# Performance work log

Hardware: AMD Instinct MI355X
Metric: run time of the kernel (lower is better)

The kernel has to match this reference:

```python
import jax, jax.numpy as jnp
import numpy as np

HEIGHT = 480
K = 16
RADIUS = 5.0 / HEIGHT


def ball_query_idx(xy, radius, k):
    """pytorch3d-style ball_query on 2D points (t-channel is zeroed in the
    original, so 3D distance == 2D distance on (x, y)).
    Returns first-k (in point-index order) neighbor indices within radius;
    slots with no neighbor are filled with the query's own index (the
    module's `-1 -> self` replacement).  xy: [B, N, 2] -> idx: [B, N, k] int32."""
    B, N, _ = xy.shape
    sq = jnp.sum(xy * xy, axis=-1)  # [B, N]
    # d2[b, i, j] = ||xy[b,i] - xy[b,j]||^2, via GEMM (no [B,N,N,2] intermediate)
    d2 = sq[:, :, None] + sq[:, None, :] - 2.0 * jnp.einsum('bnd,bmd->bnm', xy, xy)
    within = d2 < radius * radius  # [B, N, N]
    ar = jnp.arange(N, dtype=jnp.int32)
    # key = j if within else N; k smallest keys == first k neighbors in index order
    keys = jnp.where(within, ar[None, None, :], N)
    neg_top, _ = jax.lax.top_k(-keys, k)  # k smallest keys, ascending after negate
    idx = -neg_top  # [B, N, k]
    self_idx = jnp.broadcast_to(ar[None, :, None], (B, N, k))
    return jnp.where(idx < N, idx, self_idx)


def knn_gather(x, idx):
    # x: [B, N, D], idx: [B, N, k] -> [B, N, k, D]
    return jax.vmap(lambda xb, ib: xb[ib])(x, idx)


def setup_inputs() -> dict:
    key = jax.random.key(0)
    k1, k2, k3 = jax.random.split(key, 3)
    B, N = 8, 4096
    out_ch = 64
    hid = out_ch * 2          # 128
    in_ch = K * 2             # 32
    xytp = jax.random.uniform(k1, (B, N, 4), dtype=jnp.float32)
    W1 = jax.random.normal(k2, (in_ch, hid), dtype=jnp.float32) / np.sqrt(in_ch)
    b1 = jnp.zeros((hid,), dtype=jnp.float32)
    W2 = jax.random.normal(k3, (hid, out_ch), dtype=jnp.float32) / np.sqrt(hid)
    b2 = jnp.zeros((out_ch,), dtype=jnp.float32)
    return {"xytp": xytp, "W1": W1, "b1": b1, "W2": W2, "b2": b2}


def reference(xytp, W1, b1, W2, b2):
    xy = xytp[..., 1:3]  # [B, N, 2]
    # ball query runs on detached coords in the original
    idx = ball_query_idx(jax.lax.stop_gradient(xy), RADIUS, K)  # [B, N, K]
    delta = xy[:, :, None, :] - knn_gather(xy, idx)  # [B, N, K, 2]
    B, N = delta.shape[:2]
    emb = delta.reshape(B, N, K * 2)  # [B, N, 2K]
    h = jax.nn.relu(emb @ W1 + b1)
    return h @ W2 + b2  # [B, N, out_channel]
```

## Files before the change

kernel.cpp:

```cpp
#include <hip/hip_runtime.h>

#define NB    8
#define NPTS  4096
#define KNN   16
#define CG    16
#define NCC   (CG * CG)
#define PCAP  24

#define R2F ((float)((5.0 / 480.0) * (5.0 / 480.0)))
#define WIN 0.011f

__global__ __launch_bounds__(1024, 8) void k_all(
    const float4* __restrict__ xytp4, const float* __restrict__ W1,
    const float* __restrict__ b1, const float* __restrict__ W2,
    const float* __restrict__ b2, float* __restrict__ out) {
#pragma clang fp contract(off)
  __shared__ __align__(16) char smemA[32768];
  __shared__ unsigned short csrIdx[4096];
  __shared__ int offs[NCC + 1];
  __shared__ int cellcnt[NCC];
  __shared__ unsigned int plist[64 * PCAP];
  __shared__ int pcnt[64];
  __shared__ unsigned short idxposT[KNN][64];
  __shared__ float embT[32][64];

  float* csrX = (float*)smemA;
  float* csrY = (float*)(smemA + 16384);
  float(*hsT)[64] = (float(*)[64])smemA;

  const int t = threadIdx.x;
  const int p = t & 63;
  const int q = t >> 6;
  const int pbase = blockIdx.x * 64;
  const int bb = pbase & ~4095;
  const int lqbase = pbase & 4095;

  float4 Preg[4];
  int cellreg[4];
#pragma unroll
  for (int r = 0; r < 4; ++r) Preg[r] = xytp4[bb + t + 1024 * r];
  if (t < NCC) cellcnt[t] = 0;
  __syncthreads();
#pragma unroll
  for (int r = 0; r < 4; ++r) {
    int cx = min(CG - 1, max(0, (int)(Preg[r].y * (float)CG)));
    int cy = min(CG - 1, max(0, (int)(Preg[r].z * (float)CG)));
    cellreg[r] = cy * CG + cx;
    atomicAdd(&cellcnt[cellreg[r]], 1);
  }
  __syncthreads();

  if (q == 0) {
    int b4 = p * 4;
    int s0 = cellcnt[b4], s1 = cellcnt[b4 + 1], s2 = cellcnt[b4 + 2],
        s3 = cellcnt[b4 + 3];
    int tot = s0 + s1 + s2 + s3;
    int inc = tot;
#pragma unroll
    for (int d = 1; d < 64; d <<= 1) {
      int up = __shfl_up(inc, d);
      if (p >= d) inc += up;
    }
    int ex = inc - tot;
    offs[b4] = ex; offs[b4 + 1] = ex + s0;
    offs[b4 + 2] = ex + s0 + s1; offs[b4 + 3] = ex + s0 + s1 + s2;
    if (p == 63) offs[NCC] = inc;
    cellcnt[b4] = ex; cellcnt[b4 + 1] = ex + s0;
    cellcnt[b4 + 2] = ex + s0 + s1; cellcnt[b4 + 3] = ex + s0 + s1 + s2;
  }
  __syncthreads();

#pragma unroll
  for (int r = 0; r < 4; ++r) {
    int pos = atomicAdd(&cellcnt[cellreg[r]], 1);
    csrX[pos] = Preg[r].y; csrY[pos] = Preg[r].z;
    csrIdx[pos] = (unsigned short)(t + 1024 * r);
  }
  __syncthreads();

  {
    const int q0 = q * 4;
    const unsigned long long below = (1ull << p) - 1;
#pragma unroll
    for (int g = 0; g < 4; ++g) {
      int lq = q0 + g;
      float4 P = xytp4[pbase + lq];
      float xn = P.y, yn = P.z;
      float sqn = xn * xn + yn * yn;
      int cxlo = max(0, (int)((xn - WIN) * (float)CG));
      int cxhi = min(CG - 1, (int)((xn + WIN) * (float)CG));
      int cylo = max(0, (int)((yn - WIN) * (float)CG));
      int cyhi = min(CG - 1, (int)((yn + WIN) * (float)CG));
      int cnt = 0;
      for (int cy_ = cylo; cy_ <= cyhi; ++cy_)
        for (int cx_ = cxlo; cx_ <= cxhi; ++cx_) {
          int cell = cy_ * CG + cx_;
          int st = offs[cell], en = offs[cell + 1];
          for (int base = st; base < en; base += 64) {
            int e = base + p;
            bool act = e < en;
            int ee = act ? e : st;
            float cx2 = csrX[ee], cy2 = csrY[ee];
            float cs2 = cx2 * cx2 + cy2 * cy2;
            float tt = fmaf(yn, cy2, xn * cx2);
            float d = (sqn + cs2) - (tt + tt);
            bool pass = act && (d < R2F);
            unsigned long long mask = __ballot(pass);
            if (pass) {
              int slot = cnt + __popcll(mask & below);
              if (slot < PCAP)
                plist[lq * PCAP + slot] =
                    ((unsigned int)csrIdx[ee] << 12) | (unsigned int)ee;
            }
            cnt += __popcll(mask);
          }
        }
      if (p == 0) pcnt[lq] = cnt;
    }
  }
  __syncthreads();

  if (t < 64) {
    int c = min(pcnt[t], PCAP);
    unsigned int* cand = &plist[t * PCAP];
    for (int i = 1; i < c; ++i) {
      unsigned int key = cand[i];
      int j = i - 1;
      while (j >= 0 && cand[j] > key) { cand[j + 1] = cand[j]; --j; }
      cand[j + 1] = key;
    }
    unsigned short selfPos = 0;
    if (c < KNN) {
      unsigned int selfIdx = (unsigned int)(lqbase + t);
      for (int i = 0; i < c; ++i)
        if ((cand[i] >> 12) == selfIdx) { selfPos = cand[i] & 4095u; break; }
    }
    if (c > KNN) c = KNN;
    for (int k = 0; k < KNN; ++k)
      idxposT[k][t] =
          (k < c) ? (unsigned short)(cand[k] & 4095u) : selfPos;
  }
  __syncthreads();

  {
    float4 Pq = xytp4[pbase + p];
    int m = idxposT[q][p];
    embT[2 * q][p] = Pq.y - csrX[m];
    embT[2 * q + 1][p] = Pq.z - csrY[m];
  }
  __syncthreads();

  {
    const int u0 = __builtin_amdgcn_readfirstlane(q) * 8;
    float h[8];
#pragma unroll
    for (int j = 0; j < 8; ++j) h[j] = b1[u0 + j];
#pragma unroll
    for (int k = 0; k < 32; ++k) {
      float ek = embT[k][p];
      const float* __restrict__ w0 = W1 + k * 128 + u0;
#pragma unroll
      for (int j = 0; j < 8; ++j) h[j] = fmaf(ek, w0[j], h[j]);
    }
#pragma unroll
    for (int j = 0; j < 8; ++j)
      hsT[u0 + j][p] = fmaxf(h[j], 0.f);
  }
  __syncthreads();

  {
    const int o0 = __builtin_amdgcn_readfirstlane(q) * 4;
    float acc[4];
#pragma unroll
    for (int j = 0; j < 4; ++j) acc[j] = b2[o0 + j];
#pragma unroll 8
    for (int g = 0; g < 64; ++g) {
      float h0 = hsT[2 * g][p];
      float h1 = hsT[2 * g + 1][p];
      const float* __restrict__ w0 = W2 + (2 * g) * 64 + o0;
#pragma unroll
      for (int j = 0; j < 4; ++j) acc[j] = fmaf(h0, w0[j], acc[j]);
#pragma unroll
      for (int j = 0; j < 4; ++j) acc[j] = fmaf(h1, w0[64 + j], acc[j]);
    }
    *(float4*)(out + (size_t)(pbase + p) * 64 + o0) =
        make_float4(acc[0], acc[1], acc[2], acc[3]);
  }
}

extern "C" void kernel_launch(void* const* d_in, const int* in_sizes, int n_in,
                              void* d_out, int out_size, void* d_ws, size_t ws_size,
                              hipStream_t stream) {
  const float4* xytp4 = (const float4*)d_in[0];
  const float* W1 = (const float*)d_in[1];
  const float* b1 = (const float*)d_in[2];
  const float* W2 = (const float*)d_in[3];
  const float* b2 = (const float*)d_in[4];
  float* out = (float*)d_out;
  (void)d_ws; (void)ws_size;

  hipLaunchKernelGGL(k_all, dim3(512), dim3(1024), 0, stream, xytp4, W1, b1,
                     W2, b2, out);
}
```

Measured before the change: 86.65 us.

## Split grid CSR build into a separate per-batch kernel shared by all blocks

Moves the spatial grid counting, prefix scan and CSR scatter into a new kernel that runs once per batch and writes cell offsets and sorted points to workspace. The main kernel then just loads the prebuilt CSR into shared memory instead of every block rebuilding it. This removes work repeated 64 times per batch, at the cost of an extra kernel launch, a serialized 8-block build stage, and global memory round-trips.

Measured after the change: 89.45 us. 1.03x slower.

```diff
diff --git a/kernel.cpp b/kernel.cpp
--- a/kernel.cpp
+++ b/kernel.cpp
@@ -10,15 +10,75 @@
 #define R2F ((float)((5.0 / 480.0) * (5.0 / 480.0)))
 #define WIN 0.011f
 
-__global__ __launch_bounds__(1024, 8) void k_all(
-    const float4* __restrict__ xytp4, const float* __restrict__ W1,
+#define WS_CSR 0x10000
+
+__global__ __launch_bounds__(1024) void k_build(
+    const float4* __restrict__ xytp4, int* __restrict__ offs_g,
+    float4* __restrict__ csr_g) {
+#pragma clang fp contract(off)
+  __shared__ int offs[NCC + 1];
+  __shared__ int cellcnt[NCC];
+
+  const int t = threadIdx.x;
+  const int p = t & 63;
+  const int q = t >> 6;
+  const int b = blockIdx.x;
+  const int bb = b << 12;
+
+  float4 Preg[4];
+  int cellreg[4];
+#pragma unroll
+  for (int r = 0; r < 4; ++r) Preg[r] = xytp4[bb + t + 1024 * r];
+  if (t < NCC) cellcnt[t] = 0;
+  __syncthreads();
+#pragma unroll
+  for (int r = 0; r < 4; ++r) {
+    int cx = min(CG - 1, max(0, (int)(Preg[r].y * (float)CG)));
+    int cy = min(CG - 1, max(0, (int)(Preg[r].z * (float)CG)));
+    cellreg[r] = cy * CG + cx;
+    atomicAdd(&cellcnt[cellreg[r]], 1);
+  }
+  __syncthreads();
+
+  if (q == 0) {
+    int b4 = p * 4;
+    int s0 = cellcnt[b4], s1 = cellcnt[b4 + 1], s2 = cellcnt[b4 + 2],
+        s3 = cellcnt[b4 + 3];
+    int tot = s0 + s1 + s2 + s3;
+    int inc = tot;
+#pragma unroll
+    for (int d = 1; d < 64; d <<= 1) {
+      int up = __shfl_up(inc, d);
+      if (p >= d) inc += up;
+    }
+    int ex = inc - tot;
+    offs[b4] = ex; offs[b4 + 1] = ex + s0;
+    offs[b4 + 2] = ex + s0 + s1; offs[b4 + 3] = ex + s0 + s1 + s2;
+    if (p == 63) offs[NCC] = inc;
+    cellcnt[b4] = ex; cellcnt[b4 + 1] = ex + s0;
+    cellcnt[b4 + 2] = ex + s0 + s1; cellcnt[b4 + 3] = ex + s0 + s1 + s2;
+  }
+  __syncthreads();
+
+#pragma unroll
+  for (int r = 0; r < 4; ++r) {
+    int pos = atomicAdd(&cellcnt[cellreg[r]], 1);
+    csr_g[(b << 12) + pos] =
+        make_float4(Preg[r].y, Preg[r].z,
+                    __uint_as_float((unsigned)(t + 1024 * r)), 0.f);
+  }
+  if (t < NCC + 1) offs_g[b * (NCC + 1) + t] = offs[t];
+}
+
+__global__ __launch_bounds__(1024, 8) void k_main(
+    const float4* __restrict__ xytp4, const int* __restrict__ offs_g,
+    const float4* __restrict__ csr_g, const float* __restrict__ W1,
     const float* __restrict__ b1, const float* __restrict__ W2,
     const float* __restrict__ b2, float* __restrict__ out) {
 #pragma clang fp contract(off)
   __shared__ __align__(16) char smemA[32768];
   __shared__ unsigned short csrIdx[4096];
   __shared__ int offs[NCC + 1];
-  __shared__ int cellcnt[NCC];
   __shared__ unsigned int plist[64 * PCAP];
   __shared__ int pcnt[64];
   __shared__ unsigned short idxposT[KNN][64];
@@ -32,50 +92,17 @@
   const int p = t & 63;
   const int q = t >> 6;
   const int pbase = blockIdx.x * 64;
-  const int bb = pbase & ~4095;
+  const int b = pbase >> 12;
   const int lqbase = pbase & 4095;
 
-  float4 Preg[4];
-  int cellreg[4];
-#pragma unroll
-  for (int r = 0; r < 4; ++r) Preg[r] = xytp4[bb + t + 1024 * r];
-  if (t < NCC) cellcnt[t] = 0;
-  __syncthreads();
 #pragma unroll
   for (int r = 0; r < 4; ++r) {
-    int cx = min(CG - 1, max(0, (int)(Preg[r].y * (float)CG)));
-    int cy = min(CG - 1, max(0, (int)(Preg[r].z * (float)CG)));
-    cellreg[r] = cy * CG + cx;
-    atomicAdd(&cellcnt[cellreg[r]], 1);
-  }
-  __syncthreads();
-
-  if (q == 0) {
-    int b4 = p * 4;
-    int s0 = cellcnt[b4], s1 = cellcnt[b4 + 1], s2 = cellcnt[b4 + 2],
-        s3 = cellcnt[b4 + 3];
-    int tot = s0 + s1 + s2 + s3;
-    int inc = tot;
-#pragma unroll
-    for (int d = 1; d < 64; d <<= 1) {
-      int up = __shfl_up(inc, d);
-      if (p >= d) inc += up;
-    }
-    int ex = inc - tot;
-    offs[b4] = ex; offs[b4 + 1] = ex + s0;
-    offs[b4 + 2] = ex + s0 + s1; offs[b4 + 3] = ex + s0 + s1 + s2;
-    if (p == 63) offs[NCC] = inc;
-    cellcnt[b4] = ex; cellcnt[b4 + 1] = ex + s0;
-    cellcnt[b4 + 2] = ex + s0 + s1; cellcnt[b4 + 3] = ex + s0 + s1 + s2;
-  }
-  __syncthreads();
-
-#pragma unroll
-  for (int r = 0; r < 4; ++r) {
-    int pos = atomicAdd(&cellcnt[cellreg[r]], 1);
-    csrX[pos] = Preg[r].y; csrY[pos] = Preg[r].z;
-    csrIdx[pos] = (unsigned short)(t + 1024 * r);
-  }
+    int i = t + 1024 * r;
+    float4 c = csr_g[(b << 12) + i];
+    csrX[i] = c.x; csrY[i] = c.y;
+    csrIdx[i] = (unsigned short)__float_as_uint(c.z);
+  }
+  if (t < NCC + 1) offs[t] = offs_g[b * (NCC + 1) + t];
   __syncthreads();
 
   {
@@ -197,8 +224,13 @@
   const float* W2 = (const float*)d_in[3];
   const float* b2 = (const float*)d_in[4];
   float* out = (float*)d_out;
-  (void)d_ws; (void)ws_size;
-
-  hipLaunchKernelGGL(k_all, dim3(512), dim3(1024), 0, stream, xytp4, W1, b1,
-                     W2, b2, out);
+
+  char* ws = (char*)d_ws;
+  int* offs_g = (int*)ws;
+  float4* csr_g = (float4*)(ws + WS_CSR);
+
+  hipLaunchKernelGGL(k_build, dim3(8), dim3(1024), 0, stream, xytp4, offs_g,
+                     csr_g);
+  hipLaunchKernelGGL(k_main, dim3(512), dim3(1024), 0, stream, xytp4, offs_g,
+                     csr_g, W1, b1, W2, b2, out);
 }
```

## Run both MLP layers on bf16 MFMA instead of scalar FP32 FMAs

Applied to the files above, without the earlier changes.

Replaces the two per-thread FP32 FMA loops of the MLP with 16x16x32 bf16 MFMA instructions. Embeddings, weights and hidden activations are converted to bf16 on the fly, and the hidden layer is stored as a padded bf16 row-major shared tile. This is meant to cut ALU instruction count in the MLP stage. It lowers precision to bf16 inputs, which risks failing the accuracy tolerance, and it reconverts the weights from global memory in every block.

New measurement: 79.69 us. 1.09x faster.

```diff
diff --git a/kernel.cpp b/kernel.cpp
--- a/kernel.cpp
+++ b/kernel.cpp
@@ -9,6 +9,15 @@
 
 #define R2F ((float)((5.0 / 480.0) * (5.0 / 480.0)))
 #define WIN 0.011f
+
+typedef short short8 __attribute__((ext_vector_type(8)));
+typedef float f32x4 __attribute__((ext_vector_type(4)));
+
+static __device__ __forceinline__ unsigned short f2bf(float f) {
+  unsigned u = __float_as_uint(f);
+  u += 0x7FFFu + ((u >> 16) & 1u);
+  return (unsigned short)(u >> 16);
+}
 
 __global__ __launch_bounds__(1024, 8) void k_all(
     const float4* __restrict__ xytp4, const float* __restrict__ W1,
@@ -26,7 +35,8 @@
 
   float* csrX = (float*)smemA;
   float* csrY = (float*)(smemA + 16384);
-  float(*hsT)[64] = (float(*)[64])smemA;
+  unsigned short(*hs16b)[136] =
+      (unsigned short(*)[136])smemA;
 
   const int t = threadIdx.x;
   const int p = t & 63;
@@ -150,41 +160,50 @@
   }
   __syncthreads();
 
-  {
-    const int u0 = __builtin_amdgcn_readfirstlane(q) * 8;
-    float h[8];
-#pragma unroll
-    for (int j = 0; j < 8; ++j) h[j] = b1[u0 + j];
-#pragma unroll
-    for (int k = 0; k < 32; ++k) {
-      float ek = embT[k][p];
-      const float* __restrict__ w0 = W1 + k * 128 + u0;
-#pragma unroll
-      for (int j = 0; j < 8; ++j) h[j] = fmaf(ek, w0[j], h[j]);
-    }
-#pragma unroll
-    for (int j = 0; j < 8; ++j)
-      hsT[u0 + j][p] = fmaxf(h[j], 0.f);
-  }
-  __syncthreads();
-
-  {
-    const int o0 = __builtin_amdgcn_readfirstlane(q) * 4;
-    float acc[4];
-#pragma unroll
-    for (int j = 0; j < 4; ++j) acc[j] = b2[o0 + j];
-#pragma unroll 8
-    for (int g = 0; g < 64; ++g) {
-      float h0 = hsT[2 * g][p];
-      float h1 = hsT[2 * g + 1][p];
-      const float* __restrict__ w0 = W2 + (2 * g) * 64 + o0;
-#pragma unroll
-      for (int j = 0; j < 4; ++j) acc[j] = fmaf(h0, w0[j], acc[j]);
-#pragma unroll
-      for (int j = 0; j < 4; ++j) acc[j] = fmaf(h1, w0[64 + j], acc[j]);
-    }
-    *(float4*)(out + (size_t)(pbase + p) * 64 + o0) =
-        make_float4(acc[0], acc[1], acc[2], acc[3]);
+  const int lr = p & 15;
+  const int lg = p >> 4;
+
+  {
+    const int mi = q & 3;
+    const int ni0 = (q >> 2) * 2;
+    short8 a;
+#pragma unroll
+    for (int i = 0; i < 8; ++i)
+      a[i] = (short)f2bf(embT[lg * 8 + i][mi * 16 + lr]);
+#pragma unroll
+    for (int tni = 0; tni < 2; ++tni) {
+      const int u0 = (ni0 + tni) * 16;
+      short8 bfr;
+#pragma unroll
+      for (int i = 0; i < 8; ++i)
+        bfr[i] = (short)f2bf(W1[(lg * 8 + i) * 128 + u0 + lr]);
+      float bs = b1[u0 + lr];
+      f32x4 c; c[0] = bs; c[1] = bs; c[2] = bs; c[3] = bs;
+      f32x4 d = __builtin_amdgcn_mfma_f32_16x16x32_bf16(a, bfr, c, 0, 0, 0);
+#pragma unroll
+      for (int j = 0; j < 4; ++j)
+        hs16b[mi * 16 + lg * 4 + j][u0 + lr] = f2bf(fmaxf(d[j], 0.f));
+    }
+  }
+  __syncthreads();
+
+  {
+    const int mi = q >> 2;
+    const int o0 = (q & 3) * 16;
+    float bs = b2[o0 + lr];
+    f32x4 c; c[0] = bs; c[1] = bs; c[2] = bs; c[3] = bs;
+#pragma unroll
+    for (int kk = 0; kk < 4; ++kk) {
+      short8 a = *(const short8*)&hs16b[mi * 16 + lr][kk * 32 + lg * 8];
+      short8 bfr;
+#pragma unroll
+      for (int i = 0; i < 8; ++i)
+        bfr[i] = (short)f2bf(W2[(kk * 32 + lg * 8 + i) * 64 + o0 + lr]);
+      c = __builtin_amdgcn_mfma_f32_16x16x32_bf16(a, bfr, c, 0, 0, 0);
+    }
+#pragma unroll
+    for (int j = 0; j < 4; ++j)
+      out[(size_t)(pbase + mi * 16 + lg * 4 + j) * 64 + o0 + lr] = c[j];
   }
 }
 
```
